# Optimization experiments

Measured on AMD Instinct MI355X. Metric: run time of the kernel, lower is better.

Reference implementation:

```python
import jax, jax.numpy as jnp
import numpy as np
import math

B, S, D = 2, 2048, 2048
H, KV = 16, 4
HD = D // H          # 128
REP = H // KV        # 4


def setup_inputs() -> dict:
    key = jax.random.key(0)
    ks = jax.random.split(key, 6)
    x = jax.random.normal(ks[0], (B, S, D), dtype=jnp.float32)
    wq = jax.random.normal(ks[1], (D, D), dtype=jnp.float32) * (D ** -0.5)
    wk = jax.random.normal(ks[2], (KV * HD, D), dtype=jnp.float32) * (D ** -0.5)
    wv = jax.random.normal(ks[3], (KV * HD, D), dtype=jnp.float32) * (D ** -0.5)
    wo = jax.random.normal(ks[4], (D, D), dtype=jnp.float32) * (D ** -0.5)
    # RoPE frequencies: theta_i = 10000^(-2i/hd), angle = pos * theta_i
    inv_freq = 1.0 / (10000.0 ** (np.arange(0, HD, 2, dtype=np.float32) / HD))
    angles = np.arange(S, dtype=np.float32)[:, None] * inv_freq[None, :]  # [S, HD/2]
    freqs_cos = jnp.asarray(np.cos(angles), dtype=jnp.float32)
    freqs_sin = jnp.asarray(np.sin(angles), dtype=jnp.float32)
    return {"x": x, "wq": wq, "wk": wk, "wv": wv, "wo": wo,
            "freqs_cos": freqs_cos, "freqs_sin": freqs_sin}


def _rope(t, cos, sin):
    # t: [B, S, h, HD]; cos/sin: [S, HD/2]; complex multiply on (even, odd) pairs
    tr = t.reshape(*t.shape[:-1], HD // 2, 2)
    t0, t1 = tr[..., 0], tr[..., 1]
    c = cos[None, :, None, :]
    s = sin[None, :, None, :]
    o0 = t0 * c - t1 * s
    o1 = t0 * s + t1 * c
    return jnp.stack([o0, o1], axis=-1).reshape(t.shape)


def reference(x, wq, wk, wv, wo, freqs_cos, freqs_sin):
    # projections (torch Linear: y = x @ W.T)
    q = jnp.einsum('bsd,ed->bse', x, wq).reshape(B, S, H, HD)
    k = jnp.einsum('bsd,ed->bse', x, wk).reshape(B, S, KV, HD)
    v = jnp.einsum('bsd,ed->bse', x, wv).reshape(B, S, KV, HD)
    q = _rope(q, freqs_cos, freqs_sin)
    k = _rope(k, freqs_cos, freqs_sin)
    # GQA: repeat each kv head REP times -> [B, S, H, HD]
    k = jnp.repeat(k, REP, axis=2)
    v = jnp.repeat(v, REP, axis=2)
    # [B, H, S, HD]
    q = q.transpose(0, 2, 1, 3)
    k = k.transpose(0, 2, 1, 3)
    v = v.transpose(0, 2, 1, 3)
    scores = jnp.einsum('bhqd,bhkd->bhqk', q, k) * (1.0 / math.sqrt(HD))
    # faithful to torch: tril then masked_fill(scores == 0, -inf)
    scores = jnp.tril(scores)
    scores = jnp.where(scores == 0.0, -jnp.inf, scores)
    attn = jax.nn.softmax(scores, axis=-1)
    out = jnp.einsum('bhqk,bhkd->bhqd', attn, v)
    out = out.transpose(0, 2, 1, 3).reshape(B, S, D)
    return jnp.einsum('bsd,ed->bse', out, wo)
```

## Files before the change

### kernel.cpp

```cpp
#include <hip/hip_runtime.h>
#include <stdint.h>

#define B_ 2
#define S_ 2048
#define D_ 2048
#define NH 16
#define NKV 4
#define HD_ 128

typedef unsigned short u16;
typedef unsigned int u32;
typedef __attribute__((ext_vector_type(8))) __bf16 bf16x8;
typedef __attribute__((ext_vector_type(4))) float f32x4;
typedef __attribute__((ext_vector_type(16))) float f32x16;
typedef __attribute__((ext_vector_type(4))) unsigned int u32x4;
typedef __attribute__((ext_vector_type(8))) unsigned short ushort8v;

__device__ __forceinline__ u16 f2bf(float f) {
  u32 u = __builtin_bit_cast(u32, f);
  u32 r = (u + 0x7FFFu + ((u >> 16) & 1u)) >> 16;
  return (u16)r;
}
__device__ __forceinline__ float bf2f(u16 h) {
  return __builtin_bit_cast(float, ((u32)h) << 16);
}
__device__ __forceinline__ u32 cvtpk(float lo, float hi) {
  u32 r;
  asm("v_cvt_pk_bf16_f32 %0, %1, %2" : "=v"(r) : "v"(lo), "v"(hi));
  return r;
}
__device__ __forceinline__ float fexp2(float x) {
  float r;
  asm("v_exp_f32 %0, %1" : "=v"(r) : "v"(x));
  return r;
}
__device__ __forceinline__ f32x16 zero16() {
  f32x16 v;
#pragma unroll
  for (int i = 0; i < 16; ++i) v[i] = 0.f;
  return v;
}

__device__ __forceinline__ void gld_lds16(const void* g, void* l) {
  __builtin_amdgcn_global_load_lds(
      (const __attribute__((address_space(1))) void*)g,
      (__attribute__((address_space(3))) void*)l, 16, 0, 0);
}

#define QSCALE 0.12750527540095196f

__device__ __forceinline__ void cv8(const float* s, u16* d, int i) {
  const float4* sp = (const float4*)s + 2 * (size_t)i;
  float4 a = sp[0], b = sp[1];
  ushort8v o;
  o[0] = f2bf(a.x); o[1] = f2bf(a.y); o[2] = f2bf(a.z); o[3] = f2bf(a.w);
  o[4] = f2bf(b.x); o[5] = f2bf(b.y); o[6] = f2bf(b.z); o[7] = f2bf(b.w);
  *((ushort8v*)d + i) = o;
}
__global__ __launch_bounds__(256) void k_f2b_all(const float* __restrict__ x,
    const float* __restrict__ wq, const float* __restrict__ wk,
    const float* __restrict__ wv, const float* __restrict__ wo,
    u16* __restrict__ xb, u16* __restrict__ wqkv, u16* __restrict__ wob) {
  int i = blockIdx.x * 256 + threadIdx.x;
  if (i < 1048576) { cv8(x, xb, i); return; }
  i -= 1048576;
  if (i < 524288) { cv8(wq, wqkv, i); return; }
  i -= 524288;
  if (i < 131072) { cv8(wk, wqkv + 2048 * 2048, i); return; }
  i -= 131072;
  if (i < 131072) { cv8(wv, wqkv + 2560 * 2048, i); return; }
  i -= 131072;
  if (i < 524288) cv8(wo, wob, i);
}

__global__ __launch_bounds__(512, 1) void k_gemm_qkv(const u16* __restrict__ A,
    const u16* __restrict__ W, u16* __restrict__ Qd, u16* __restrict__ Kd,
    u16* __restrict__ Vd, const float* __restrict__ fc,
    const float* __restrict__ fs, int K) {
  __shared__ char lds[2][49152];
  const int tid = threadIdx.x, lane = tid & 63, wave = tid >> 6;
  const int wm = wave >> 2, wn = wave & 3;
  const int m0 = blockIdx.x * 256, n0 = blockIdx.y * 128;
  const size_t Kb2 = (size_t)K * 2;
  f32x4 acc[8][2];
#pragma unroll
  for (int mi = 0; mi < 8; ++mi)
#pragma unroll
    for (int ni = 0; ni < 2; ++ni) acc[mi][ni] = f32x4{0.f, 0.f, 0.f, 0.f};
  int rA[4], cA[4], rB[2], cB[2];
#pragma unroll
  for (int j = 0; j < 4; ++j) {
    int p = j * 8192 + tid * 16;
    int o = p ^ (((p >> 7) & 7) << 4);
    rA[j] = o >> 7; cA[j] = o & 127;
  }
#pragma unroll
  for (int j = 0; j < 2; ++j) {
    int p = j * 8192 + tid * 16;
    int o = p ^ (((p >> 7) & 7) << 4);
    rB[j] = o >> 7; cB[j] = o & 127;
  }
  auto stage = [&](int t) {
    char* dst = &lds[t & 1][0];
    const char* As = (const char*)A + (size_t)t * 128;
    const char* Ws = (const char*)W + (size_t)t * 128;
#pragma unroll
    for (int j = 0; j < 4; ++j)
      gld_lds16(As + (size_t)(m0 + rA[j]) * Kb2 + cA[j], dst + j * 8192 + tid * 16);
#pragma unroll
    for (int j = 0; j < 2; ++j)
      gld_lds16(Ws + (size_t)(n0 + rB[j]) * Kb2 + cB[j], dst + 32768 + j * 8192 + tid * 16);
  };
  stage(0);
  __syncthreads();
  const int nt = K >> 6;
  for (int t = 0; t < nt; ++t) {
    if (t + 1 < nt) stage(t + 1);
    const char* buf = &lds[t & 1][0];
#pragma unroll
    for (int kk = 0; kk < 2; ++kk) {
      const int cb = kk * 64 + ((lane >> 4) << 4);
      bf16x8 af[8], bfr[2];
#pragma unroll
      for (int mi = 0; mi < 8; ++mi) {
        int r = wm * 128 + mi * 16 + (lane & 15);
        af[mi] = *(const bf16x8*)(buf + (r << 7) + (cb ^ ((r & 7) << 4)));
      }
#pragma unroll
      for (int ni = 0; ni < 2; ++ni) {
        int r = wn * 32 + ni * 16 + (lane & 15);
        bfr[ni] = *(const bf16x8*)(buf + 32768 + (r << 7) + (cb ^ ((r & 7) << 4)));
      }
      __builtin_amdgcn_s_setprio(1);
#pragma unroll
      for (int mi = 0; mi < 8; ++mi)
#pragma unroll
        for (int ni = 0; ni < 2; ++ni)
          acc[mi][ni] = __builtin_amdgcn_mfma_f32_16x16x32_bf16(af[mi], bfr[ni], acc[mi][ni], 0, 0, 0);
      __builtin_amdgcn_s_setprio(0);
    }
    __syncthreads();
  }
  const int seg = blockIdx.y;
  const int bb = m0 >> 11;
  if (seg < 20) {
    const bool isQ = (seg < 16);
    const int h = isQ ? seg : seg - 16;
    u16* dstB = isQ ? (Qd + ((size_t)(bb * NH + h)) * S_ * HD_)
                    : (Kd + ((size_t)(bb * NKV + h)) * S_ * HD_);
    const float sc = isQ ? QSCALE : 1.0f;
#pragma unroll
    for (int ni = 0; ni < 2; ++ni) {
      const int c = (n0 + wn * 32 + ni * 16 + (lane & 15)) & 127;
      const int j = c >> 1;
#pragma unroll
      for (int mi = 0; mi < 8; ++mi)
#pragma unroll
        for (int r = 0; r < 4; ++r) {
          const int m = m0 + wm * 128 + mi * 16 + ((lane >> 4) << 2) + r;
          const int s = m & 2047;
          float val = acc[mi][ni][r];
          float par = __shfl_xor(val, 1);
          float cs = fc[s * 64 + j], sn = fs[s * 64 + j];
          float outv = (c & 1) ? (par * sn + val * cs) : (val * cs - par * sn);
          dstB[(size_t)s * HD_ + c] = f2bf(outv * sc);
        }
    }
  } else {
    const int h = seg - 20;
    u16* dstB = Vd + ((size_t)(bb * NKV + h)) * S_ * HD_;
#pragma unroll
    for (int ni = 0; ni < 2; ++ni) {
      const int c = (n0 + wn * 32 + ni * 16 + (lane & 15)) & 127;
#pragma unroll
      for (int mi = 0; mi < 8; ++mi)
#pragma unroll
        for (int r = 0; r < 4; ++r) {
          const int m = m0 + wm * 128 + mi * 16 + ((lane >> 4) << 2) + r;
          const int s = m & 2047;
          dstB[(size_t)s * HD_ + c] = f2bf(acc[mi][ni][r]);
        }
    }
  }
}

__global__ __launch_bounds__(512, 1) void k_gemm_out(const u16* __restrict__ A,
    const u16* __restrict__ W, float* __restrict__ C, int N, int K) {
  __shared__ char lds[2][49152];
  const int tid = threadIdx.x, lane = tid & 63, wave = tid >> 6;
  const int wm = wave >> 2, wn = wave & 3;
  const int m0 = blockIdx.x * 256, n0 = blockIdx.y * 128;
  const size_t Kb2 = (size_t)K * 2;
  f32x4 acc[8][2];
#pragma unroll
  for (int mi = 0; mi < 8; ++mi)
#pragma unroll
    for (int ni = 0; ni < 2; ++ni) acc[mi][ni] = f32x4{0.f, 0.f, 0.f, 0.f};
  int rA[4], cA[4], rB[2], cB[2];
#pragma unroll
  for (int j = 0; j < 4; ++j) {
    int p = j * 8192 + tid * 16;
    int o = p ^ (((p >> 7) & 7) << 4);
    rA[j] = o >> 7; cA[j] = o & 127;
  }
#pragma unroll
  for (int j = 0; j < 2; ++j) {
    int p = j * 8192 + tid * 16;
    int o = p ^ (((p >> 7) & 7) << 4);
    rB[j] = o >> 7; cB[j] = o & 127;
  }
  auto stage = [&](int t) {
    char* dst = &lds[t & 1][0];
    const char* As = (const char*)A + (size_t)t * 128;
    const char* Ws = (const char*)W + (size_t)t * 128;
#pragma unroll
    for (int j = 0; j < 4; ++j)
      gld_lds16(As + (size_t)(m0 + rA[j]) * Kb2 + cA[j], dst + j * 8192 + tid * 16);
#pragma unroll
    for (int j = 0; j < 2; ++j)
      gld_lds16(Ws + (size_t)(n0 + rB[j]) * Kb2 + cB[j], dst + 32768 + j * 8192 + tid * 16);
  };
  stage(0);
  __syncthreads();
  const int nt = K >> 6;
  for (int t = 0; t < nt; ++t) {
    if (t + 1 < nt) stage(t + 1);
    const char* buf = &lds[t & 1][0];
#pragma unroll
    for (int kk = 0; kk < 2; ++kk) {
      const int cb = kk * 64 + ((lane >> 4) << 4);
      bf16x8 af[8], bfr[2];
#pragma unroll
      for (int mi = 0; mi < 8; ++mi) {
        int r = wm * 128 + mi * 16 + (lane & 15);
        af[mi] = *(const bf16x8*)(buf + (r << 7) + (cb ^ ((r & 7) << 4)));
      }
#pragma unroll
      for (int ni = 0; ni < 2; ++ni) {
        int r = wn * 32 + ni * 16 + (lane & 15);
        bfr[ni] = *(const bf16x8*)(buf + 32768 + (r << 7) + (cb ^ ((r & 7) << 4)));
      }
      __builtin_amdgcn_s_setprio(1);
#pragma unroll
      for (int mi = 0; mi < 8; ++mi)
#pragma unroll
        for (int ni = 0; ni < 2; ++ni)
          acc[mi][ni] = __builtin_amdgcn_mfma_f32_16x16x32_bf16(af[mi], bfr[ni], acc[mi][ni], 0, 0, 0);
      __builtin_amdgcn_s_setprio(0);
    }
    __syncthreads();
  }
#pragma unroll
  for (int mi = 0; mi < 8; ++mi)
#pragma unroll
    for (int ni = 0; ni < 2; ++ni) {
      const int n = n0 + wn * 32 + ni * 16 + (lane & 15);
#pragma unroll
      for (int r = 0; r < 4; ++r) {
        const int m = m0 + wm * 128 + mi * 16 + ((lane >> 4) << 2) + r;
        C[(size_t)m * N + n] = acc[mi][ni][r];
      }
    }
}

__global__ __launch_bounds__(256, 2) void k_attn(const u16* __restrict__ Q,
    const u16* __restrict__ Kt, const u16* __restrict__ Vt, u16* __restrict__ O) {
  __shared__ char kls[2][16384];
  __shared__ char vls[2][16384];
  const int h = blockIdx.x, b = blockIdx.y;
  const int z = blockIdx.z;
  const int qtb = (z < 8) ? (15 - z) : (z - 8);
  const int tid = threadIdx.x, lane = tid & 63, wave = tid >> 6;
  const int ql = lane & 31, g = lane >> 5;
  const int kvh = h >> 2;
  const u16* Qb = Q + ((size_t)(b * NH + h)) * S_ * HD_;
  const u16* Kb = Kt + ((size_t)(b * NKV + kvh)) * S_ * HD_;
  const u16* Vb = Vt + ((size_t)(b * NKV + kvh)) * S_ * HD_;
  const int q0 = qtb * 128, qw0 = q0 + wave * 32;
  const int qme = qw0 + ql;
  int kRowS[4], kColS[4];
#pragma unroll
  for (int j = 0; j < 4; ++j) {
    int plin = j * 4096 + tid * 16;
    int o = plin ^ (((plin >> 8) & 7) << 4);
    kRowS[j] = o >> 8;
    kColS[j] = o & 255;
  }
  const int kp = tid & 31, hb = (tid >> 5) * 16;
  auto loadV = [&](int tn, u32* vr0, u32* vr1) {
    const u16* vp = Vb + (size_t)(tn * 64 + 2 * kp) * HD_ + hb;
    const u32* r0 = (const u32*)vp;
    const u32* r1 = (const u32*)(vp + HD_);
#pragma unroll
    for (int wd = 0; wd < 8; ++wd) { vr0[wd] = r0[wd]; vr1[wd] = r1[wd]; }
  };
  auto writeV = [&](char* vn, const u32* vr0, const u32* vr1) {
#pragma unroll
    for (int wd = 0; wd < 8; ++wd) {
      u32 v0 = vr0[wd], v1 = vr1[wd];
      u32 lo = (v0 & 0xFFFFu) | (v1 << 16);
      u32 hi = (v0 >> 16) | (v1 & 0xFFFF0000u);
      int hd0 = hb + 2 * wd, hd1 = hd0 + 1;
      *(u32*)(vn + hd0 * 128 + ((4 * kp) ^ ((hd0 & 7) << 4))) = lo;
      *(u32*)(vn + hd1 * 128 + ((4 * kp) ^ ((hd1 & 7) << 4))) = hi;
    }
  };

#pragma unroll
  for (int j = 0; j < 4; ++j)
    gld_lds16((const char*)Kb + (size_t)kRowS[j] * 256 + kColS[j],
              &kls[0][0] + j * 4096 + wave * 1024);
  u32 pv0[8], pv1[8];
  loadV(0, pv0, pv1);
  bf16x8 qf[8];
#pragma unroll
  for (int kk = 0; kk < 8; ++kk)
    qf[kk] = *(const bf16x8*)(Qb + (size_t)qme * HD_ + kk * 16 + g * 8);
  writeV(&vls[0][0], pv0, pv1);
  __syncthreads();

  f32x16 oacc[4];
#pragma unroll
  for (int th = 0; th < 4; ++th) oacc[th] = zero16();
  float mrun = -1e30f, lrun = 0.0f;
  const int nt = 2 * qtb + 2;

  int cur = 0;
  for (int t = 0; t < nt; ++t) {
    const int kv0 = t * 64;
    const bool haveNext = (t + 1 < nt);
    u32 vr0[8], vr1[8];
    if (haveNext) {
      const int kvn = kv0 + 64;
#pragma unroll
      for (int j = 0; j < 4; ++j)
        gld_lds16((const char*)Kb + (size_t)(kvn + kRowS[j]) * 256 + kColS[j],
                  &kls[cur ^ 1][0] + j * 4096 + wave * 1024);
      loadV(t + 1, vr0, vr1);
    }
    if (kv0 <= qw0 + 31) {
      const char* kcur = &kls[cur][0];
      const char* vcur = &vls[cur][0];
      f32x16 c0 = zero16(), c1 = zero16();
      __builtin_amdgcn_s_setprio(1);
#pragma unroll
      for (int kk = 0; kk < 8; ++kk) {
        const int sw = (kk * 32 + 16 * g) ^ ((ql & 7) << 4);
        bf16x8 kf0 = *(const bf16x8*)(kcur + (ql << 8) + sw);
        bf16x8 kf1 = *(const bf16x8*)(kcur + ((32 + ql) << 8) + sw);
        c0 = __builtin_amdgcn_mfma_f32_32x32x16_bf16(kf0, qf[kk], c0, 0, 0, 0);
        c1 = __builtin_amdgcn_mfma_f32_32x32x16_bf16(kf1, qf[kk], c1, 0, 0, 0);
      }
      __builtin_amdgcn_s_setprio(0);
      const bool diag = (kv0 + 63 > qw0);
      float mt = -1e30f;
      if (diag) {
#pragma unroll
        for (int r = 0; r < 16; ++r) {
          float s0 = c0[r], s1 = c1[r];
          int kb = kv0 + (r & 3) + ((r >> 2) << 3) + 4 * g;
          if (kb > qme) s0 = -1e30f;
          if (kb + 32 > qme) s1 = -1e30f;
          c0[r] = s0; c1[r] = s1;
          mt = fmaxf(mt, fmaxf(s0, s1));
        }
      } else {
#pragma unroll
        for (int r = 0; r < 16; ++r)
          mt = fmaxf(mt, fmaxf(c0[r], c1[r]));
      }
      mt = fmaxf(mt, __shfl_xor(mt, 32));
      if (!__all(mt <= mrun + 8.0f)) {
        float mnew = fmaxf(mrun, mt);
        float alpha = fexp2(mrun - mnew);
        lrun *= alpha;
        mrun = mnew;
#pragma unroll
        for (int r = 0; r < 16; ++r) {
          float av = __shfl(alpha, 36 * g + (r & 3) + ((r >> 2) << 3));
          oacc[0][r] *= av; oacc[1][r] *= av;
          oacc[2][r] *= av; oacc[3][r] *= av;
        }
      }
      float lt = 0.0f;
#pragma unroll
      for (int r = 0; r < 16; ++r) {
        float p0 = fexp2(c0[r] - mrun);
        float p1 = fexp2(c1[r] - mrun);
        c0[r] = p0; c1[r] = p1;
        lt += p0 + p1;
      }
      lt += __shfl_xor(lt, 32);
      lrun += lt;
      u32 paw[4][4];
#pragma unroll
      for (int a = 0; a < 2; ++a) {
        {
          u32 X = cvtpk(c0[8 * a + 0], c0[8 * a + 1]);
          u32 Y = cvtpk(c0[8 * a + 2], c0[8 * a + 3]);
          u32 Z = cvtpk(c0[8 * a + 4], c0[8 * a + 5]);
          u32 W = cvtpk(c0[8 * a + 6], c0[8 * a + 7]);
          u32 S1 = g ? X : Z, S2 = g ? Y : W;
          u32 R1 = (u32)__shfl_xor((int)S1, 32), R2 = (u32)__shfl_xor((int)S2, 32);
          paw[a][0] = g ? R1 : X; paw[a][1] = g ? R2 : Y;
          paw[a][2] = g ? Z : R1; paw[a][3] = g ? W : R2;
        }
        {
          u32 X = cvtpk(c1[8 * a + 0], c1[8 * a + 1]);
          u32 Y = cvtpk(c1[8 * a + 2], c1[8 * a + 3]);
          u32 Z = cvtpk(c1[8 * a + 4], c1[8 * a + 5]);
          u32 W = cvtpk(c1[8 * a + 6], c1[8 * a + 7]);
          u32 S1 = g ? X : Z, S2 = g ? Y : W;
          u32 R1 = (u32)__shfl_xor((int)S1, 32), R2 = (u32)__shfl_xor((int)S2, 32);
          paw[2 + a][0] = g ? R1 : X; paw[2 + a][1] = g ? R2 : Y;
          paw[2 + a][2] = g ? Z : R1; paw[2 + a][3] = g ? W : R2;
        }
      }
      __builtin_amdgcn_s_setprio(1);
#pragma unroll
      for (int ks = 0; ks < 4; ++ks) {
        bf16x8 pf = __builtin_bit_cast(bf16x8,
            u32x4{paw[ks][0], paw[ks][1], paw[ks][2], paw[ks][3]});
        const int cb = (32 * ks + 16 * g) ^ ((ql & 7) << 4);
#pragma unroll
        for (int th = 0; th < 4; ++th) {
          bf16x8 vf = *(const bf16x8*)(vcur + ((th * 32 + ql) << 7) + cb);
          oacc[th] = __builtin_amdgcn_mfma_f32_32x32x16_bf16(pf, vf, oacc[th], 0, 0, 0);
        }
      }
      __builtin_amdgcn_s_setprio(0);
    }
    if (haveNext) writeV(&vls[cur ^ 1][0], vr0, vr1);
    __syncthreads();
    cur ^= 1;
  }
#pragma unroll
  for (int r = 0; r < 16; ++r) {
    float lr = __shfl(lrun, 36 * g + (r & 3) + ((r >> 2) << 3));
    float li = 1.0f / lr;
    int q = qw0 + (r & 3) + ((r >> 2) << 3) + 4 * g;
    size_t rowo = (size_t)(b * S_ + q) * D_ + h * HD_ + ql;
#pragma unroll
    for (int th = 0; th < 4; ++th)
      O[rowo + 32 * th] = f2bf(oacc[th][r] * li);
  }
}

extern "C" void kernel_launch(void* const* d_in, const int* in_sizes, int n_in,
                              void* d_out, int out_size, void* d_ws, size_t ws_size,
                              hipStream_t stream) {
  const float* x  = (const float*)d_in[0];
  const float* wq = (const float*)d_in[1];
  const float* wk = (const float*)d_in[2];
  const float* wv = (const float*)d_in[3];
  const float* wo = (const float*)d_in[4];
  const float* fc = (const float*)d_in[5];
  const float* fs = (const float*)d_in[6];
  float* out = (float*)d_out;
  char* ws = (char*)d_ws;
  const size_t MB = 1ull << 20;
  u16* xb   = (u16*)(ws);
  u16* wqkv = (u16*)(ws + 16 * MB);
  u16* wob  = (u16*)(ws + 28 * MB);
  u16* Qb   = (u16*)(ws + 36 * MB);
  u16* Kb   = (u16*)(ws + 52 * MB);
  u16* Vb   = (u16*)(ws + 56 * MB);
  u16* attb = (u16*)(ws);

  k_f2b_all<<<dim3(9216), dim3(256), 0, stream>>>(x, wq, wk, wv, wo, xb, wqkv, wob);

  k_gemm_qkv<<<dim3(16, 24), dim3(512), 0, stream>>>(xb, wqkv, Qb, Kb, Vb, fc, fs, D_);

  k_attn<<<dim3(NH, B_, 16), dim3(256), 0, stream>>>(Qb, Kb, Vb, attb);

  k_gemm_out<<<dim3(16, 16), dim3(512), 0, stream>>>(attb, wob, out, D_, D_);
}
```

Before: 207.9 us.

## Load fp32 weights directly in GEMMs and convert to bf16 from LDS

```diff
diff --git a/kernel.cpp b/kernel.cpp
--- a/kernel.cpp
+++ b/kernel.cpp
@@ -49,67 +49,55 @@
 
 #define QSCALE 0.12750527540095196f
 
-__device__ __forceinline__ void cv8(const float* s, u16* d, int i) {
-  const float4* sp = (const float4*)s + 2 * (size_t)i;
+__global__ __launch_bounds__(256) void k_f2b_x(const float* __restrict__ x,
+                                               u16* __restrict__ xb) {
+  int i = blockIdx.x * 256 + threadIdx.x;
+  const float4* sp = (const float4*)x + 2 * (size_t)i;
   float4 a = sp[0], b = sp[1];
   ushort8v o;
   o[0] = f2bf(a.x); o[1] = f2bf(a.y); o[2] = f2bf(a.z); o[3] = f2bf(a.w);
   o[4] = f2bf(b.x); o[5] = f2bf(b.y); o[6] = f2bf(b.z); o[7] = f2bf(b.w);
-  *((ushort8v*)d + i) = o;
-}
-__global__ __launch_bounds__(256) void k_f2b_all(const float* __restrict__ x,
-    const float* __restrict__ wq, const float* __restrict__ wk,
-    const float* __restrict__ wv, const float* __restrict__ wo,
-    u16* __restrict__ xb, u16* __restrict__ wqkv, u16* __restrict__ wob) {
-  int i = blockIdx.x * 256 + threadIdx.x;
-  if (i < 1048576) { cv8(x, xb, i); return; }
-  i -= 1048576;
-  if (i < 524288) { cv8(wq, wqkv, i); return; }
-  i -= 524288;
-  if (i < 131072) { cv8(wk, wqkv + 2048 * 2048, i); return; }
-  i -= 131072;
-  if (i < 131072) { cv8(wv, wqkv + 2560 * 2048, i); return; }
-  i -= 131072;
-  if (i < 524288) cv8(wo, wob, i);
+  *((ushort8v*)xb + i) = o;
 }
 
 __global__ __launch_bounds__(512, 1) void k_gemm_qkv(const u16* __restrict__ A,
-    const u16* __restrict__ W, u16* __restrict__ Qd, u16* __restrict__ Kd,
+    const float* __restrict__ Wq, const float* __restrict__ Wk,
+    const float* __restrict__ Wv, u16* __restrict__ Qd, u16* __restrict__ Kd,
     u16* __restrict__ Vd, const float* __restrict__ fc,
     const float* __restrict__ fs, int K) {
-  __shared__ char lds[2][49152];
+  __shared__ char lds[2][65536];
   const int tid = threadIdx.x, lane = tid & 63, wave = tid >> 6;
   const int wm = wave >> 2, wn = wave & 3;
   const int m0 = blockIdx.x * 256, n0 = blockIdx.y * 128;
+  const int by = blockIdx.y;
   const size_t Kb2 = (size_t)K * 2;
+  const float* Wrow0 = (by < 16) ? Wq + (size_t)n0 * K
+                      : (by < 20) ? Wk + (size_t)(n0 - 2048) * K
+                                  : Wv + (size_t)(n0 - 2560) * K;
   f32x4 acc[8][2];
 #pragma unroll
   for (int mi = 0; mi < 8; ++mi)
 #pragma unroll
     for (int ni = 0; ni < 2; ++ni) acc[mi][ni] = f32x4{0.f, 0.f, 0.f, 0.f};
-  int rA[4], cA[4], rB[2], cB[2];
+  int rA[4], cA[4], rB[4], cB[4];
 #pragma unroll
   for (int j = 0; j < 4; ++j) {
     int p = j * 8192 + tid * 16;
     int o = p ^ (((p >> 7) & 7) << 4);
     rA[j] = o >> 7; cA[j] = o & 127;
-  }
-#pragma unroll
-  for (int j = 0; j < 2; ++j) {
-    int p = j * 8192 + tid * 16;
-    int o = p ^ (((p >> 7) & 7) << 4);
-    rB[j] = o >> 7; cB[j] = o & 127;
+    int ob = p ^ (((p >> 8) & 15) << 4);
+    rB[j] = ob >> 8; cB[j] = ob & 255;
   }
   auto stage = [&](int t) {
     char* dst = &lds[t & 1][0];
     const char* As = (const char*)A + (size_t)t * 128;
-    const char* Ws = (const char*)W + (size_t)t * 128;
+    const char* Ws = (const char*)Wrow0 + (size_t)t * 256;
 #pragma unroll
     for (int j = 0; j < 4; ++j)
       gld_lds16(As + (size_t)(m0 + rA[j]) * Kb2 + cA[j], dst + j * 8192 + tid * 16);
 #pragma unroll
-    for (int j = 0; j < 2; ++j)
-      gld_lds16(Ws + (size_t)(n0 + rB[j]) * Kb2 + cB[j], dst + 32768 + j * 8192 + tid * 16);
+    for (int j = 0; j < 4; ++j)
+      gld_lds16(Ws + (size_t)rB[j] * K * 4 + cB[j], dst + 32768 + j * 8192 + tid * 16);
   };
   stage(0);
   __syncthreads();
@@ -129,7 +117,14 @@
 #pragma unroll
       for (int ni = 0; ni < 2; ++ni) {
         int r = wn * 32 + ni * 16 + (lane & 15);
-        bfr[ni] = *(const bf16x8*)(buf + 32768 + (r << 7) + (cb ^ ((r & 7) << 4)));
+        int sw = (r & 15) << 4;
+        int b0 = 2 * cb;
+        const char* bbp = buf + 32768 + (r << 8);
+        f32x4 lo = *(const f32x4*)(bbp + (b0 ^ sw));
+        f32x4 hi = *(const f32x4*)(bbp + ((b0 + 16) ^ sw));
+        bfr[ni] = __builtin_bit_cast(bf16x8,
+            u32x4{cvtpk(lo[0], lo[1]), cvtpk(lo[2], lo[3]),
+                  cvtpk(hi[0], hi[1]), cvtpk(hi[2], hi[3])});
       }
       __builtin_amdgcn_s_setprio(1);
 #pragma unroll
@@ -141,7 +136,7 @@
     }
     __syncthreads();
   }
-  const int seg = blockIdx.y;
+  const int seg = by;
   const int bb = m0 >> 11;
   if (seg < 20) {
     const bool isQ = (seg < 16);
@@ -185,40 +180,37 @@
 }
 
 __global__ __launch_bounds__(512, 1) void k_gemm_out(const u16* __restrict__ A,
-    const u16* __restrict__ W, float* __restrict__ C, int N, int K) {
-  __shared__ char lds[2][49152];
+    const float* __restrict__ W, float* __restrict__ C, int N, int K) {
+  __shared__ char lds[2][65536];
   const int tid = threadIdx.x, lane = tid & 63, wave = tid >> 6;
   const int wm = wave >> 2, wn = wave & 3;
   const int m0 = blockIdx.x * 256, n0 = blockIdx.y * 128;
   const size_t Kb2 = (size_t)K * 2;
+  const float* Wrow0 = W + (size_t)n0 * K;
   f32x4 acc[8][2];
 #pragma unroll
   for (int mi = 0; mi < 8; ++mi)
 #pragma unroll
     for (int ni = 0; ni < 2; ++ni) acc[mi][ni] = f32x4{0.f, 0.f, 0.f, 0.f};
-  int rA[4], cA[4], rB[2], cB[2];
+  int rA[4], cA[4], rB[4], cB[4];
 #pragma unroll
   for (int j = 0; j < 4; ++j) {
     int p = j * 8192 + tid * 16;
     int o = p ^ (((p >> 7) & 7) << 4);
     rA[j] = o >> 7; cA[j] = o & 127;
-  }
-#pragma unroll
-  for (int j = 0; j < 2; ++j) {
-    int p = j * 8192 + tid * 16;
-    int o = p ^ (((p >> 7) & 7) << 4);
-    rB[j] = o >> 7; cB[j] = o & 127;
+    int ob = p ^ (((p >> 8) & 15) << 4);
+    rB[j] = ob >> 8; cB[j] = ob & 255;
   }
   auto stage = [&](int t) {
     char* dst = &lds[t & 1][0];
     const char* As = (const char*)A + (size_t)t * 128;
-    const char* Ws = (const char*)W + (size_t)t * 128;
+    const char* Ws = (const char*)Wrow0 + (size_t)t * 256;
 #pragma unroll
     for (int j = 0; j < 4; ++j)
       gld_lds16(As + (size_t)(m0 + rA[j]) * Kb2 + cA[j], dst + j * 8192 + tid * 16);
 #pragma unroll
-    for (int j = 0; j < 2; ++j)
-      gld_lds16(Ws + (size_t)(n0 + rB[j]) * Kb2 + cB[j], dst + 32768 + j * 8192 + tid * 16);
+    for (int j = 0; j < 4; ++j)
+      gld_lds16(Ws + (size_t)rB[j] * K * 4 + cB[j], dst + 32768 + j * 8192 + tid * 16);
   };
   stage(0);
   __syncthreads();
@@ -238,7 +230,14 @@
 #pragma unroll
       for (int ni = 0; ni < 2; ++ni) {
         int r = wn * 32 + ni * 16 + (lane & 15);
-        bfr[ni] = *(const bf16x8*)(buf + 32768 + (r << 7) + (cb ^ ((r & 7) << 4)));
+        int sw = (r & 15) << 4;
+        int b0 = 2 * cb;
+        const char* bbp = buf + 32768 + (r << 8);
+        f32x4 lo = *(const f32x4*)(bbp + (b0 ^ sw));
+        f32x4 hi = *(const f32x4*)(bbp + ((b0 + 16) ^ sw));
+        bfr[ni] = __builtin_bit_cast(bf16x8,
+            u32x4{cvtpk(lo[0], lo[1]), cvtpk(lo[2], lo[3]),
+                  cvtpk(hi[0], hi[1]), cvtpk(hi[2], hi[3])});
       }
       __builtin_amdgcn_s_setprio(1);
 #pragma unroll
@@ -282,7 +281,7 @@
 #pragma unroll
   for (int j = 0; j < 4; ++j) {
     int plin = j * 4096 + tid * 16;
-    int o = plin ^ (((plin >> 8) & 7) << 4);
+    int o = plin ^ (((plin >> 8) & 15) << 4);
     kRowS[j] = o >> 8;
     kColS[j] = o & 255;
   }
@@ -345,7 +344,7 @@
       __builtin_amdgcn_s_setprio(1);
 #pragma unroll
       for (int kk = 0; kk < 8; ++kk) {
-        const int sw = (kk * 32 + 16 * g) ^ ((ql & 7) << 4);
+        const int sw = (kk * 32 + 16 * g) ^ ((ql & 15) << 4);
         bf16x8 kf0 = *(const bf16x8*)(kcur + (ql << 8) + sw);
         bf16x8 kf1 = *(const bf16x8*)(kcur + ((32 + ql) << 8) + sw);
         c0 = __builtin_amdgcn_mfma_f32_32x32x16_bf16(kf0, qf[kk], c0, 0, 0, 0);
@@ -460,18 +459,17 @@
   char* ws = (char*)d_ws;
   const size_t MB = 1ull << 20;
   u16* xb   = (u16*)(ws);
-  u16* wqkv = (u16*)(ws + 16 * MB);
-  u16* wob  = (u16*)(ws + 28 * MB);
   u16* Qb   = (u16*)(ws + 36 * MB);
   u16* Kb   = (u16*)(ws + 52 * MB);
   u16* Vb   = (u16*)(ws + 56 * MB);
   u16* attb = (u16*)(ws);
 
-  k_f2b_all<<<dim3(9216), dim3(256), 0, stream>>>(x, wq, wk, wv, wo, xb, wqkv, wob);
-
-  k_gemm_qkv<<<dim3(16, 24), dim3(512), 0, stream>>>(xb, wqkv, Qb, Kb, Vb, fc, fs, D_);
+  k_f2b_x<<<dim3(4096), dim3(256), 0, stream>>>(x, xb);
+
+  k_gemm_qkv<<<dim3(16, 24), dim3(512), 0, stream>>>(xb, wq, wk, wv, Qb, Kb, Vb,
+                                                     fc, fs, D_);
 
   k_attn<<<dim3(NH, B_, 16), dim3(256), 0, stream>>>(Qb, Kb, Vb, attb);
 
-  k_gemm_out<<<dim3(16, 16), dim3(512), 0, stream>>>(attb, wob, out, D_, D_);
-}
+  k_gemm_out<<<dim3(16, 16), dim3(512), 0, stream>>>(attb, wo, out, D_, D_);
+}
```

Measured after the change: 223.3 us. 7.4% more time.
